# Kernel tuning notes

Measured on AMD Instinct MI355X. Metric: run time of the kernel, lower is better.

## Reference

```python
import math
import jax, jax.numpy as jnp
import numpy as np

D_MODEL = 1024
NUM_HEADS = 16
MAX_SEQ_LEN = 2048
THETA = 10000.0


def setup_inputs() -> dict:
    key = jax.random.key(0)
    ks = jax.random.split(key, 5)
    B, S, D = 2, 2048, D_MODEL
    std = math.sqrt(2.0 / (D + D))
    x = jax.random.normal(ks[0], (B, S, D), dtype=jnp.float32)
    wq = jax.random.normal(ks[1], (D, D), dtype=jnp.float32) * std
    wk = jax.random.normal(ks[2], (D, D), dtype=jnp.float32) * std
    wv = jax.random.normal(ks[3], (D, D), dtype=jnp.float32) * std
    wo = jax.random.normal(ks[4], (D, D), dtype=jnp.float32) * std
    return {"x": x, "wq": wq, "wk": wk, "wv": wv, "wo": wo}


def _rope_tables(seq_len: int, d_k: int):
    # angles[i, k] = i / theta^(2k/d_k), k over d_k//2 pairs
    inv_freq = 1.0 / (THETA ** (jnp.arange(0, d_k, 2, dtype=jnp.float32) / d_k))
    angles = jnp.arange(seq_len, dtype=jnp.float32)[:, None] * inv_freq[None, :]  # [S, d_k/2]
    return jnp.cos(angles), jnp.sin(angles)


def _apply_rope(x, cos, sin):
    # x: [..., S, d_k]; cos/sin: [S, d_k/2], broadcast over leading dims
    x_even = x[..., ::2]
    x_odd = x[..., 1::2]
    r_even = x_even * cos - x_odd * sin
    r_odd = x_even * sin + x_odd * cos
    return jnp.stack([r_even, r_odd], axis=-1).reshape(x.shape)


def reference(x, wq, wk, wv, wo):
    B, S, D = x.shape
    H = NUM_HEADS
    dk = D // H

    def split_heads(t):  # [B,S,D] -> [B,H,S,dk]
        return t.reshape(B, S, H, dk).transpose(0, 2, 1, 3)

    Q = split_heads(x @ wq.T)
    K = split_heads(x @ wk.T)
    V = split_heads(x @ wv.T)

    cos, sin = _rope_tables(S, dk)
    Q = _apply_rope(Q, cos, sin)
    K = _apply_rope(K, cos, sin)

    scores = jnp.einsum('bhqd,bhkd->bhqk', Q, K) / jnp.sqrt(jnp.float32(dk))
    mask = jnp.tril(jnp.ones((S, S), dtype=bool))  # causal: q can attend k <= q
    neg_inf = jnp.float32(-jnp.inf)
    scores = jnp.where(mask, scores, neg_inf)
    m = jnp.max(scores, axis=-1, keepdims=True)
    m = jnp.where(jnp.isinf(m), jnp.zeros_like(m), m)
    exp_scores = jnp.exp(scores - m)
    exp_scores = jnp.where(mask, exp_scores, 0.0)
    attn = exp_scores / (jnp.sum(exp_scores, axis=-1, keepdims=True) + 1e-9)
    out = jnp.einsum('bhqk,bhkd->bhqd', attn, V)  # [B,H,S,dk]
    out = out.transpose(0, 2, 1, 3).reshape(B, S, D)
    return out @ wo.T
```

## Files before the change

kernel.cpp:

```cpp
#include <hip/hip_runtime.h>
#include <stdint.h>

typedef unsigned short u16;
typedef unsigned int u32;
typedef __bf16 bf16x8 __attribute__((ext_vector_type(8)));
typedef float f32x4 __attribute__((ext_vector_type(4)));
typedef unsigned short u16x8 __attribute__((ext_vector_type(8)));

#define D_MODEL 1024
#define SEQ 2048
#define NH 16
#define DK 64
#define NROWS 4096

static __device__ __forceinline__ u16 f2bf(float f) {
  u32 u = __float_as_uint(f);
  u = (u + 0x7FFFu + ((u >> 16) & 1u)) >> 16;
  return (u16)u;
}
static __device__ __forceinline__ float bf2f(u16 h) {
  return __uint_as_float(((u32)h) << 16);
}
static __device__ __forceinline__ f32x4 mfma16(bf16x8 a, bf16x8 b, f32x4 c) {
  return __builtin_amdgcn_mfma_f32_16x16x32_bf16(a, b, c, 0, 0, 0);
}
static __device__ __forceinline__ void gload16(const void* g, void* l) {
  __builtin_amdgcn_global_load_lds(
      (const __attribute__((address_space(1))) void*)g,
      (__attribute__((address_space(3))) void*)l, 16, 0, 0);
}

static __device__ __forceinline__ float xor32_max(float x) {
#if __has_builtin(__builtin_amdgcn_permlane32_swap)
  u32 a = __float_as_uint(x), b = a;
  auto pr = __builtin_amdgcn_permlane32_swap(a, b, false, false);
  return fmaxf(__uint_as_float(pr[0]), __uint_as_float(pr[1]));
#else
  return fmaxf(x, __shfl_xor(x, 32));
#endif
}
static __device__ __forceinline__ float xor32_add(float x) {
#if __has_builtin(__builtin_amdgcn_permlane32_swap)
  u32 a = __float_as_uint(x), b = a;
  auto pr = __builtin_amdgcn_permlane32_swap(a, b, false, false);
  return __uint_as_float(pr[0]) + __uint_as_float(pr[1]);
#else
  return x + __shfl_xor(x, 32);
#endif
}

__global__ __launch_bounds__(256) void k_cast(
    const float* __restrict__ x, const float* __restrict__ wq,
    const float* __restrict__ wk, const float* __restrict__ wv,
    const float* __restrict__ wo, u16* __restrict__ xb, u16* __restrict__ wqb,
    u16* __restrict__ wkb, u16* __restrict__ wvb, u16* __restrict__ wob) {
  size_t e = ((size_t)blockIdx.x * 256 + threadIdx.x) * 8;
  const float* s;
  u16* d;
  size_t off;
  if (e < (size_t)NROWS * D_MODEL) {
    s = x; d = xb; off = e;
  } else {
    size_t r = e - (size_t)NROWS * D_MODEL;
    unsigned wi = (unsigned)(r >> 20);
    off = r & 1048575u;
    s = wi == 0 ? wq : wi == 1 ? wk : wi == 2 ? wv : wo;
    d = wi == 0 ? wqb : wi == 1 ? wkb : wi == 2 ? wvb : wob;
  }
  float4 a = *(const float4*)(s + off);
  float4 b = *(const float4*)(s + off + 4);
  u16x8 o;
  o[0] = f2bf(a.x); o[1] = f2bf(a.y); o[2] = f2bf(a.z); o[3] = f2bf(a.w);
  o[4] = f2bf(b.x); o[5] = f2bf(b.y); o[6] = f2bf(b.z); o[7] = f2bf(b.w);
  *(u16x8*)(d + off) = o;
}

__global__ __launch_bounds__(256) void k_tab(float* __restrict__ ct, float* __restrict__ st) {
  int i = blockIdx.x * 256 + threadIdx.x;
  int s = i >> 5, p = i & 31;
  double ang = (double)s * pow(10000.0, -(double)p / 32.0);
  ct[i] = (float)cos(ang);
  st[i] = (float)sin(ang);
}

template <bool MULTI, bool OUTF32>
__global__ __launch_bounds__(256, 1) void k_gemm(
    const u16* __restrict__ A, const u16* __restrict__ B0,
    const u16* __restrict__ B1, const u16* __restrict__ B2,
    u16* __restrict__ Cb, float* __restrict__ Cf, int ldc) {
  constexpr int K = 1024;
  const int mb = blockIdx.x, nb = blockIdx.y;
  const int tid = threadIdx.x;
  const int lane = tid & 63, w = tid >> 6;
  const int lq = lane & 15, lg = lane >> 4;
  const int wm = w >> 1, wn = w & 1;
  __shared__ __align__(16) u16 As[128 * 32];
  __shared__ __align__(16) u16 Bs[128 * 32];

  const u16* Bp;
  if (MULTI) {
    int sel = nb >> 3;
    Bp = sel == 0 ? B0 : (sel == 1 ? B1 : B2);
  } else {
    Bp = B0;
  }
  int nloc = MULTI ? (nb & 7) * 128 : nb * 128;
  const char* Ab = (const char*)A + (size_t)mb * 128 * 2048;
  const char* Bb = (const char*)Bp + (size_t)nloc * 2048;

  const int srow = tid >> 2;
  const int scb = (tid & 3) * 16;

  f32x4 zero4 = {0.f, 0.f, 0.f, 0.f};
  f32x4 acc[4][4];
#pragma unroll
  for (int i = 0; i < 4; ++i)
#pragma unroll
    for (int j = 0; j < 4; ++j) acc[i][j] = zero4;

  for (int k0 = 0; k0 < K; k0 += 32) {
#pragma unroll
    for (int c = 0; c < 2; ++c) {
      int o = c * 4096 + tid * 16;
      const char* ga = Ab + (size_t)(c * 64 + srow) * 2048 + k0 * 2 + scb;
      const char* gb = Bb + (size_t)(c * 64 + srow) * 2048 + k0 * 2 + scb;
      gload16(ga, (char*)As + o);
      gload16(gb, (char*)Bs + o);
    }
    __syncthreads();
    bf16x8 af[4], bfr[4];
#pragma unroll
    for (int i = 0; i < 4; ++i) {
      af[i] = *(const bf16x8*)((const char*)As + (wm * 64 + i * 16 + lq) * 64 + lg * 16);
      bfr[i] = *(const bf16x8*)((const char*)Bs + (wn * 64 + i * 16 + lq) * 64 + lg * 16);
    }
#pragma unroll
    for (int i = 0; i < 4; ++i)
#pragma unroll
      for (int j = 0; j < 4; ++j) acc[i][j] = mfma16(af[i], bfr[j], acc[i][j]);
    __syncthreads();
  }

#pragma unroll
  for (int i = 0; i < 4; ++i) {
#pragma unroll
    for (int r = 0; r < 4; ++r) {
      size_t rowg = (size_t)(mb * 128 + wm * 64 + i * 16 + lg * 4 + r);
#pragma unroll
      for (int j = 0; j < 4; ++j) {
        int colg = nb * 128 + wn * 64 + j * 16 + lq;
        if (OUTF32)
          Cf[rowg * ldc + colg] = acc[i][j][r];
        else
          Cb[rowg * ldc + colg] = f2bf(acc[i][j][r]);
      }
    }
  }
}

__global__ __launch_bounds__(256) void k_rope(const u16* __restrict__ qkv,
                                              const float* __restrict__ ct,
                                              const float* __restrict__ st,
                                              u16* __restrict__ qh, u16* __restrict__ kh) {
  int gi = blockIdx.x * 256 + threadIdx.x;
  int row = gi >> 7;
  int col = (gi & 127) << 3;
  int h = col >> 6, d0 = col & 63;
  int b = row >> 11, s = row & 2047;
  const int srcoff = blockIdx.y ? 1024 : 0;
  const float qs = blockIdx.y ? 1.0f : 0.18033688011112042f;
  u16x8 v = *(const u16x8*)(qkv + (size_t)row * 3072 + srcoff + col);
  const float* cp = ct + s * 32 + (d0 >> 1);
  const float* sp = st + s * 32 + (d0 >> 1);
  u16x8 o;
#pragma unroll
  for (int i = 0; i < 4; ++i) {
    float ev = bf2f(v[2 * i]), od = bf2f(v[2 * i + 1]);
    float c = cp[i], sn = sp[i];
    o[2 * i] = f2bf((ev * c - od * sn) * qs);
    o[2 * i + 1] = f2bf((ev * sn + od * c) * qs);
  }
  u16* dst = blockIdx.y ? kh : qh;
  *(u16x8*)(dst + (((size_t)(b * 16 + h) * SEQ + s) << 6) + d0) = o;
}

__global__ __launch_bounds__(256) void k_vtrans(const u16* __restrict__ qkv,
                                                u16* __restrict__ vt) {
  __shared__ __align__(16) u16 t[64][72];
  int sb = blockIdx.x, bh = blockIdx.y;
  int b = bh >> 4, h = bh & 15;
  int tid = threadIdx.x;
#pragma unroll
  for (int c = 0; c < 2; ++c) {
    int o = tid * 8 + c * 2048;
    int r = o >> 6, d = o & 63;
    u16x8 v = *(const u16x8*)(qkv + (size_t)(b * SEQ + sb * 64 + r) * 3072 + 2048 + h * 64 + d);
    *(u16x8*)&t[r][d] = v;
  }
  __syncthreads();
#pragma unroll
  for (int c = 0; c < 2; ++c) {
    int o = tid * 8 + c * 2048;
    int d = o >> 6, si = o & 63;
    u16x8 v;
#pragma unroll
    for (int j = 0; j < 8; ++j) v[j] = t[si + j][d];
    *(u16x8*)(vt + ((size_t)bh * 64 + d) * SEQ + sb * 64 + si) = v;
  }
}

static __device__ __forceinline__ void attn_tile(
    const u16* Kl, const u16* Vl, u16* Plw, int k0, int qrow, int lq, int lg,
    bf16x8 qf0, bf16x8 qf1, float& m_run, float& l_run, f32x4* accO, bool masked) {
  f32x4 zero4 = {0.f, 0.f, 0.f, 0.f};
  f32x4 sa[4];
  sa[0] = zero4; sa[1] = zero4; sa[2] = zero4; sa[3] = zero4;
  __builtin_amdgcn_s_setprio(1);
#pragma unroll
  for (int kt = 0; kt < 4; ++kt) {
    int krow = kt * 16 + lq;
    int base = krow * 128 + lg * 16;
    int swz = (krow & 7) << 4;
    bf16x8 kf0 = *(const bf16x8*)((const char*)Kl + (base ^ swz));
    bf16x8 kf1 = *(const bf16x8*)((const char*)Kl + ((base + 64) ^ swz));
    sa[kt] = mfma16(kf0, qf0, sa[kt]);
    sa[kt] = mfma16(kf1, qf1, sa[kt]);
  }
  __builtin_amdgcn_s_setprio(0);

  float p[16];
#pragma unroll
  for (int kt = 0; kt < 4; ++kt)
#pragma unroll
    for (int r = 0; r < 4; ++r) p[kt * 4 + r] = sa[kt][r];
  if (masked) {
#pragma unroll
    for (int kt = 0; kt < 4; ++kt)
#pragma unroll
      for (int r = 0; r < 4; ++r) {
        int key = k0 + kt * 16 + lg * 4 + r;
        if (key > qrow) p[kt * 4 + r] = -1e30f;
      }
  }
  float x0 = fmaxf(p[0], p[1]), x1 = fmaxf(p[2], p[3]);
  float x2 = fmaxf(p[4], p[5]), x3 = fmaxf(p[6], p[7]);
  float x4 = fmaxf(p[8], p[9]), x5 = fmaxf(p[10], p[11]);
  float x6 = fmaxf(p[12], p[13]), x7 = fmaxf(p[14], p[15]);
  x0 = fmaxf(x0, x1); x2 = fmaxf(x2, x3); x4 = fmaxf(x4, x5); x6 = fmaxf(x6, x7);
  x0 = fmaxf(x0, x2); x4 = fmaxf(x4, x6);
  float pm = fmaxf(x0, x4);
  pm = fmaxf(pm, __shfl_xor(pm, 16));
  pm = xor32_max(pm);
  const bool resc = __any(pm > m_run + 8.0f);
  float mnew = resc ? fmaxf(m_run, pm) : m_run;
#pragma unroll
  for (int i = 0; i < 16; ++i) p[i] = __builtin_amdgcn_exp2f(p[i] - mnew);
  float s0 = p[0] + p[1], s1 = p[2] + p[3], s2 = p[4] + p[5], s3 = p[6] + p[7];
  float s4 = p[8] + p[9], s5 = p[10] + p[11], s6 = p[12] + p[13], s7 = p[14] + p[15];
  s0 += s1; s2 += s3; s4 += s5; s6 += s7;
  s0 += s2; s4 += s6;
  float rs = s0 + s4;
  rs += __shfl_xor(rs, 16);
  rs = xor32_add(rs);
  if (resc) {
    float alpha = __builtin_amdgcn_exp2f(m_run - mnew);
    l_run = l_run * alpha + rs;
    m_run = mnew;
#pragma unroll
    for (int r = 0; r < 4; ++r) {
      float ar = __shfl(alpha, lg * 4 + r);
#pragma unroll
      for (int dt = 0; dt < 4; ++dt) accO[dt][r] *= ar;
    }
  } else {
    l_run += rs;
  }

  {
    int swz = (lq & 7) << 4;
#pragma unroll
    for (int kt = 0; kt < 4; ++kt) {
      u32 w0, w1;
      asm("v_cvt_pk_bf16_f32 %0, %1, %2"
          : "=v"(w0) : "v"(p[kt * 4 + 0]), "v"(p[kt * 4 + 1]));
      asm("v_cvt_pk_bf16_f32 %0, %1, %2"
          : "=v"(w1) : "v"(p[kt * 4 + 2]), "v"(p[kt * 4 + 3]));
      int a0 = (lq * 128 + (kt * 16 + lg * 4) * 2) ^ swz;
      int a1 = (lq * 128 + (kt * 16 + lg * 4 + 2) * 2) ^ swz;
      *(u32*)((char*)Plw + a0) = w0;
      *(u32*)((char*)Plw + a1) = w1;
    }
  }
  {
    int swz = (lq & 7) << 4;
    bf16x8 pa0 = *(const bf16x8*)((const char*)Plw + ((lq * 128 + lg * 16) ^ swz));
    bf16x8 pa1 = *(const bf16x8*)((const char*)Plw + ((lq * 128 + 64 + lg * 16) ^ swz));
    __builtin_amdgcn_s_setprio(1);
#pragma unroll
    for (int dt = 0; dt < 4; ++dt) {
      int vrow = dt * 16 + lq;
      int vb = vrow * 128 + lg * 16;
      int vs = (vrow & 7) << 4;
      bf16x8 v0 = *(const bf16x8*)((const char*)Vl + (vb ^ vs));
      bf16x8 v1 = *(const bf16x8*)((const char*)Vl + ((vb + 64) ^ vs));
      accO[dt] = mfma16(pa0, v0, accO[dt]);
      accO[dt] = mfma16(pa1, v1, accO[dt]);
    }
    __builtin_amdgcn_s_setprio(0);
  }
}

__global__ __launch_bounds__(256, 2) void k_attn(const u16* __restrict__ qh,
                                                 const u16* __restrict__ kh,
                                                 const u16* __restrict__ vt,
                                                 u16* __restrict__ ao) {
  const int qb1 = (int)blockIdx.x;
  const int qb2 = 31 - qb1;
  const int bh = blockIdx.y;
  const int tid = threadIdx.x;
  const int w = tid >> 6;
  const int lane = tid & 63;
  const int lq = lane & 15;
  const int lg = lane >> 4;

  __shared__ __align__(16) u16 Kd[2][2][64 * 64];
  __shared__ __align__(16) u16 Vd[2][2][64 * 64];
  __shared__ __align__(16) u16 Pl[4][16 * 64];

  const int qtop1 = qb1 * 64 + w * 16;
  const int qtop2 = qb2 * 64 + w * 16;
  const int qrow1 = qtop1 + lq;
  const int qrow2 = qtop2 + lq;

  const u16* qp1 = qh + ((size_t)bh * SEQ + qrow1) * DK + lg * 8;
  const u16* qp2 = qh + ((size_t)bh * SEQ + qrow2) * DK + lg * 8;
  bf16x8 qa0 = *(const bf16x8*)qp1;
  bf16x8 qa1 = *(const bf16x8*)(qp1 + 32);
  bf16x8 qc0 = *(const bf16x8*)qp2;
  bf16x8 qc1 = *(const bf16x8*)(qp2 + 32);

  f32x4 zero4 = {0.f, 0.f, 0.f, 0.f};
  f32x4 acc1[4], acc2[4];
#pragma unroll
  for (int dt = 0; dt < 4; ++dt) { acc1[dt] = zero4; acc2[dt] = zero4; }
  float m1 = -1e30f, l1 = 0.f, m2 = -1e30f, l2 = 0.f;

  const int nt1 = qb1 + 1;
  const int nt2 = qb2 + 1;
  const int NIT = (nt2 + 1) >> 1;

  const char* kb_ = (const char*)kh + (size_t)bh * SEQ * 128;
  const char* vb_ = (const char*)vt + (size_t)bh * DK * 4096;

#pragma unroll
  for (int s = 0; s < 2; ++s)
#pragma unroll
    for (int pass = 0; pass < 2; ++pass) {
      int chunk = pass * 256 + tid;
      int srow = chunk >> 3;
      int colb = ((chunk & 7) * 16) ^ ((srow & 7) << 4);
      gload16(kb_ + (size_t)(s * 64 + srow) * 128 + colb,
              (char*)Kd[0][s] + chunk * 16);
      gload16(vb_ + (size_t)srow * 4096 + (s * 64) * 2 + colb,
              (char*)Vd[0][s] + chunk * 16);
    }
  __syncthreads();

  for (int it = 0; it < NIT; ++it) {
    const int cur = it & 1;
    if (it + 1 < NIT) {
      int kb0 = (it + 1) * 128;
#pragma unroll
      for (int s = 0; s < 2; ++s)
#pragma unroll
        for (int pass = 0; pass < 2; ++pass) {
          int chunk = pass * 256 + tid;
          int srow = chunk >> 3;
          int colb = ((chunk & 7) * 16) ^ ((srow & 7) << 4);
          gload16(kb_ + (size_t)(kb0 + s * 64 + srow) * 128 + colb,
                  (char*)Kd[cur ^ 1][s] + chunk * 16);
          gload16(vb_ + (size_t)srow * 4096 + (kb0 + s * 64) * 2 + colb,
                  (char*)Vd[cur ^ 1][s] + chunk * 16);
        }
    }
#pragma unroll
    for (int s = 0; s < 2; ++s) {
      const int tsub = it * 2 + s;
      const int k0 = tsub * 64;
      if (tsub < nt1)
        attn_tile(Kd[cur][s], Vd[cur][s], Pl[w], k0, qrow1, lq, lg, qa0, qa1,
                  m1, l1, acc1, tsub == nt1 - 1);
      if (tsub < nt2)
        attn_tile(Kd[cur][s], Vd[cur][s], Pl[w], k0, qrow2, lq, lg, qc0, qc1,
                  m2, l2, acc2, tsub == nt2 - 1);
    }
    __syncthreads();
  }

  const int b = bh >> 4, h = bh & 15;
#pragma unroll
  for (int r = 0; r < 4; ++r) {
    float lr = __shfl(l1, lg * 4 + r);
    float inv = 1.f / (lr + 1e-9f);
    int qq = qtop1 + lg * 4 + r;
    u16* orow = ao + ((size_t)b * SEQ + qq) * D_MODEL + h * DK;
#pragma unroll
    for (int dt = 0; dt < 4; ++dt) orow[dt * 16 + lq] = f2bf(acc1[dt][r] * inv);
  }
#pragma unroll
  for (int r = 0; r < 4; ++r) {
    float lr = __shfl(l2, lg * 4 + r);
    float inv = 1.f / (lr + 1e-9f);
    int qq = qtop2 + lg * 4 + r;
    u16* orow = ao + ((size_t)b * SEQ + qq) * D_MODEL + h * DK;
#pragma unroll
    for (int dt = 0; dt < 4; ++dt) orow[dt * 16 + lq] = f2bf(acc2[dt][r] * inv);
  }
}

extern "C" void kernel_launch(void* const* d_in, const int* in_sizes, int n_in,
                              void* d_out, int out_size, void* d_ws, size_t ws_size,
                              hipStream_t stream) {
  const float* x = (const float*)d_in[0];
  const float* wq = (const float*)d_in[1];
  const float* wk = (const float*)d_in[2];
  const float* wv = (const float*)d_in[3];
  const float* wo = (const float*)d_in[4];
  float* out = (float*)d_out;
  char* ws = (char*)d_ws;

  u16* xb   = (u16*)(ws + 0);
  u16* wqb  = (u16*)(ws + 8388608);
  u16* wkb  = (u16*)(ws + 10485760);
  u16* wvb  = (u16*)(ws + 12582912);
  u16* wob  = (u16*)(ws + 14680064);
  u16* qkv  = (u16*)(ws + 16777216);
  u16* qhb  = (u16*)(ws + 41943040);
  u16* khb  = (u16*)(ws + 50331648);
  u16* vtb  = (u16*)(ws + 58720256);
  u16* aob  = (u16*)(ws + 67108864);
  float* ct = (float*)(ws + 75497472);
  float* st = (float*)(ws + 75759616);

  k_cast<<<4096, 256, 0, stream>>>(x, wq, wk, wv, wo, xb, wqb, wkb, wvb, wob);
  k_tab<<<256, 256, 0, stream>>>(ct, st);
  k_gemm<true, false><<<dim3(32, 24), 256, 0, stream>>>(xb, wqb, wkb, wvb, qkv, nullptr, 3072);
  k_rope<<<dim3(2048, 2), 256, 0, stream>>>(qkv, ct, st, qhb, khb);
  k_vtrans<<<dim3(32, 32), 256, 0, stream>>>(qkv, vtb);
  k_attn<<<dim3(16, 32), 256, 0, stream>>>(qhb, khb, vtb, aob);
  k_gemm<false, true><<<dim3(32, 8), 256, 0, stream>>>(aob, wob, nullptr, nullptr, nullptr, out, 1024);
}
```

Measured before the change: 126.2 us.

## Fuse RoPE and V transpose into QKV GEMM epilogue

The QKV projection GEMM now applies RoPE (with the Q scale) directly in its epilogue and writes Q/K in head-major layout. V is transposed through shared memory and written straight to the V^T buffer. This removes the intermediate qkv buffer along with the separate rope and vtrans kernels, saving two launches and a full write and read of qkv. The cost is extra LDS (a 128x136 transpose tile), strided scalar bf16 stores for Q/K, and a cos/sin table packed into float2.

```diff
diff --git a/kernel.cpp b/kernel.cpp
--- a/kernel.cpp
+++ b/kernel.cpp
@@ -75,19 +75,18 @@
   *(u16x8*)(d + off) = o;
 }
 
-__global__ __launch_bounds__(256) void k_tab(float* __restrict__ ct, float* __restrict__ st) {
+__global__ __launch_bounds__(256) void k_tab(float2* __restrict__ cs) {
   int i = blockIdx.x * 256 + threadIdx.x;
   int s = i >> 5, p = i & 31;
   double ang = (double)s * pow(10000.0, -(double)p / 32.0);
-  ct[i] = (float)cos(ang);
-  st[i] = (float)sin(ang);
-}
-
-template <bool MULTI, bool OUTF32>
-__global__ __launch_bounds__(256, 1) void k_gemm(
+  cs[i] = make_float2((float)cos(ang), (float)sin(ang));
+}
+
+__global__ __launch_bounds__(256, 1) void k_gemmqkv(
     const u16* __restrict__ A, const u16* __restrict__ B0,
     const u16* __restrict__ B1, const u16* __restrict__ B2,
-    u16* __restrict__ Cb, float* __restrict__ Cf, int ldc) {
+    const float2* __restrict__ cs, u16* __restrict__ qh,
+    u16* __restrict__ kh, u16* __restrict__ vt) {
   constexpr int K = 1024;
   const int mb = blockIdx.x, nb = blockIdx.y;
   const int tid = threadIdx.x;
@@ -96,15 +95,11 @@
   const int wm = w >> 1, wn = w & 1;
   __shared__ __align__(16) u16 As[128 * 32];
   __shared__ __align__(16) u16 Bs[128 * 32];
-
-  const u16* Bp;
-  if (MULTI) {
-    int sel = nb >> 3;
-    Bp = sel == 0 ? B0 : (sel == 1 ? B1 : B2);
-  } else {
-    Bp = B0;
-  }
-  int nloc = MULTI ? (nb & 7) * 128 : nb * 128;
+  __shared__ __align__(16) u16 Tr[128][136];
+
+  const int sel = nb >> 3;
+  const u16* Bp = sel == 0 ? B0 : (sel == 1 ? B1 : B2);
+  const int nloc = (nb & 7) * 128;
   const char* Ab = (const char*)A + (size_t)mb * 128 * 2048;
   const char* Bb = (const char*)Bp + (size_t)nloc * 2048;
 
@@ -141,6 +136,103 @@
     __syncthreads();
   }
 
+  if (sel < 2) {
+    u16* dst = sel ? kh : qh;
+    const float qs = sel ? 1.0f : 0.18033688011112042f;
+    const bool oddl = (lane & 1) != 0;
+#pragma unroll
+    for (int i = 0; i < 4; ++i) {
+#pragma unroll
+      for (int r = 0; r < 4; ++r) {
+        int rowg = mb * 128 + wm * 64 + i * 16 + lg * 4 + r;
+        int s = rowg & 2047, b = rowg >> 11;
+        const float2* csrow = cs + s * 32;
+#pragma unroll
+        for (int j = 0; j < 4; ++j) {
+          int colL = nloc + wn * 64 + j * 16 + lq;
+          float v = acc[i][j][r];
+          float pv = __shfl_xor(v, 1);
+          float2 c2 = csrow[(colL & 63) >> 1];
+          float t = pv * c2.y;
+          float res = (v * c2.x + (oddl ? t : -t)) * qs;
+          int h = colL >> 6, d = colL & 63;
+          dst[((size_t)(b * 16 + h) * 2048 + s) * 64 + d] = f2bf(res);
+        }
+      }
+    }
+  } else {
+#pragma unroll
+    for (int i = 0; i < 4; ++i)
+#pragma unroll
+      for (int j = 0; j < 4; ++j)
+#pragma unroll
+        for (int r = 0; r < 4; ++r) {
+          int cb = wn * 64 + j * 16 + lq;
+          int rb = wm * 64 + i * 16 + lg * 4 + r;
+          Tr[cb][rb] = f2bf(acc[i][j][r]);
+        }
+    __syncthreads();
+    const int b = mb >> 4;
+    const int s0 = (mb & 15) * 128 + (tid & 1) * 64;
+    const int d128 = tid >> 1;
+    const int h = (nb & 7) * 2 + (d128 >> 6);
+    const int d = d128 & 63;
+    u16* vrow = vt + ((size_t)(b * 16 + h) * 64 + d) * 2048 + s0;
+    const u16* trow = &Tr[d128][(tid & 1) * 64];
+#pragma unroll
+    for (int c = 0; c < 8; ++c)
+      *(u16x8*)(vrow + c * 8) = *(const u16x8*)(trow + c * 8);
+  }
+}
+
+__global__ __launch_bounds__(256, 1) void k_gemm(
+    const u16* __restrict__ A, const u16* __restrict__ B0,
+    float* __restrict__ Cf, int ldc) {
+  constexpr int K = 1024;
+  const int mb = blockIdx.x, nb = blockIdx.y;
+  const int tid = threadIdx.x;
+  const int lane = tid & 63, w = tid >> 6;
+  const int lq = lane & 15, lg = lane >> 4;
+  const int wm = w >> 1, wn = w & 1;
+  __shared__ __align__(16) u16 As[128 * 32];
+  __shared__ __align__(16) u16 Bs[128 * 32];
+
+  const char* Ab = (const char*)A + (size_t)mb * 128 * 2048;
+  const char* Bb = (const char*)B0 + (size_t)(nb * 128) * 2048;
+
+  const int srow = tid >> 2;
+  const int scb = (tid & 3) * 16;
+
+  f32x4 zero4 = {0.f, 0.f, 0.f, 0.f};
+  f32x4 acc[4][4];
+#pragma unroll
+  for (int i = 0; i < 4; ++i)
+#pragma unroll
+    for (int j = 0; j < 4; ++j) acc[i][j] = zero4;
+
+  for (int k0 = 0; k0 < K; k0 += 32) {
+#pragma unroll
+    for (int c = 0; c < 2; ++c) {
+      int o = c * 4096 + tid * 16;
+      const char* ga = Ab + (size_t)(c * 64 + srow) * 2048 + k0 * 2 + scb;
+      const char* gb = Bb + (size_t)(c * 64 + srow) * 2048 + k0 * 2 + scb;
+      gload16(ga, (char*)As + o);
+      gload16(gb, (char*)Bs + o);
+    }
+    __syncthreads();
+    bf16x8 af[4], bfr[4];
+#pragma unroll
+    for (int i = 0; i < 4; ++i) {
+      af[i] = *(const bf16x8*)((const char*)As + (wm * 64 + i * 16 + lq) * 64 + lg * 16);
+      bfr[i] = *(const bf16x8*)((const char*)Bs + (wn * 64 + i * 16 + lq) * 64 + lg * 16);
+    }
+#pragma unroll
+    for (int i = 0; i < 4; ++i)
+#pragma unroll
+      for (int j = 0; j < 4; ++j) acc[i][j] = mfma16(af[i], bfr[j], acc[i][j]);
+    __syncthreads();
+  }
+
 #pragma unroll
   for (int i = 0; i < 4; ++i) {
 #pragma unroll
@@ -149,63 +241,9 @@
 #pragma unroll
       for (int j = 0; j < 4; ++j) {
         int colg = nb * 128 + wn * 64 + j * 16 + lq;
-        if (OUTF32)
-          Cf[rowg * ldc + colg] = acc[i][j][r];
-        else
-          Cb[rowg * ldc + colg] = f2bf(acc[i][j][r]);
+        Cf[rowg * ldc + colg] = acc[i][j][r];
       }
     }
-  }
-}
-
-__global__ __launch_bounds__(256) void k_rope(const u16* __restrict__ qkv,
-                                              const float* __restrict__ ct,
-                                              const float* __restrict__ st,
-                                              u16* __restrict__ qh, u16* __restrict__ kh) {
-  int gi = blockIdx.x * 256 + threadIdx.x;
-  int row = gi >> 7;
-  int col = (gi & 127) << 3;
-  int h = col >> 6, d0 = col & 63;
-  int b = row >> 11, s = row & 2047;
-  const int srcoff = blockIdx.y ? 1024 : 0;
-  const float qs = blockIdx.y ? 1.0f : 0.18033688011112042f;
-  u16x8 v = *(const u16x8*)(qkv + (size_t)row * 3072 + srcoff + col);
-  const float* cp = ct + s * 32 + (d0 >> 1);
-  const float* sp = st + s * 32 + (d0 >> 1);
-  u16x8 o;
-#pragma unroll
-  for (int i = 0; i < 4; ++i) {
-    float ev = bf2f(v[2 * i]), od = bf2f(v[2 * i + 1]);
-    float c = cp[i], sn = sp[i];
-    o[2 * i] = f2bf((ev * c - od * sn) * qs);
-    o[2 * i + 1] = f2bf((ev * sn + od * c) * qs);
-  }
-  u16* dst = blockIdx.y ? kh : qh;
-  *(u16x8*)(dst + (((size_t)(b * 16 + h) * SEQ + s) << 6) + d0) = o;
-}
-
-__global__ __launch_bounds__(256) void k_vtrans(const u16* __restrict__ qkv,
-                                                u16* __restrict__ vt) {
-  __shared__ __align__(16) u16 t[64][72];
-  int sb = blockIdx.x, bh = blockIdx.y;
-  int b = bh >> 4, h = bh & 15;
-  int tid = threadIdx.x;
-#pragma unroll
-  for (int c = 0; c < 2; ++c) {
-    int o = tid * 8 + c * 2048;
-    int r = o >> 6, d = o & 63;
-    u16x8 v = *(const u16x8*)(qkv + (size_t)(b * SEQ + sb * 64 + r) * 3072 + 2048 + h * 64 + d);
-    *(u16x8*)&t[r][d] = v;
-  }
-  __syncthreads();
-#pragma unroll
-  for (int c = 0; c < 2; ++c) {
-    int o = tid * 8 + c * 2048;
-    int d = o >> 6, si = o & 63;
-    u16x8 v;
-#pragma unroll
-    for (int j = 0; j < 8; ++j) v[j] = t[si + j][d];
-    *(u16x8*)(vt + ((size_t)bh * 64 + d) * SEQ + sb * 64 + si) = v;
   }
 }
 
@@ -429,24 +467,20 @@
   float* out = (float*)d_out;
   char* ws = (char*)d_ws;
 
-  u16* xb   = (u16*)(ws + 0);
-  u16* wqb  = (u16*)(ws + 8388608);
-  u16* wkb  = (u16*)(ws + 10485760);
-  u16* wvb  = (u16*)(ws + 12582912);
-  u16* wob  = (u16*)(ws + 14680064);
-  u16* qkv  = (u16*)(ws + 16777216);
-  u16* qhb  = (u16*)(ws + 41943040);
-  u16* khb  = (u16*)(ws + 50331648);
-  u16* vtb  = (u16*)(ws + 58720256);
-  u16* aob  = (u16*)(ws + 67108864);
-  float* ct = (float*)(ws + 75497472);
-  float* st = (float*)(ws + 75759616);
+  u16* xb    = (u16*)(ws + 0);
+  u16* wqb   = (u16*)(ws + 8388608);
+  u16* wkb   = (u16*)(ws + 10485760);
+  u16* wvb   = (u16*)(ws + 12582912);
+  u16* wob   = (u16*)(ws + 14680064);
+  u16* qhb   = (u16*)(ws + 41943040);
+  u16* khb   = (u16*)(ws + 50331648);
+  u16* vtb   = (u16*)(ws + 58720256);
+  u16* aob   = (u16*)(ws + 67108864);
+  float2* cs = (float2*)(ws + 75497472);
 
   k_cast<<<4096, 256, 0, stream>>>(x, wq, wk, wv, wo, xb, wqb, wkb, wvb, wob);
-  k_tab<<<256, 256, 0, stream>>>(ct, st);
-  k_gemm<true, false><<<dim3(32, 24), 256, 0, stream>>>(xb, wqb, wkb, wvb, qkv, nullptr, 3072);
-  k_rope<<<dim3(2048, 2), 256, 0, stream>>>(qkv, ct, st, qhb, khb);
-  k_vtrans<<<dim3(32, 32), 256, 0, stream>>>(qkv, vtb);
+  k_tab<<<256, 256, 0, stream>>>(cs);
+  k_gemmqkv<<<dim3(32, 24), 256, 0, stream>>>(xb, wqb, wkb, wvb, cs, qhb, khb, vtb);
   k_attn<<<dim3(16, 32), 256, 0, stream>>>(qhb, khb, vtb, aob);
-  k_gemm<false, true><<<dim3(32, 8), 256, 0, stream>>>(aob, wob, nullptr, nullptr, nullptr, out, 1024);
-}
+  k_gemm<<<dim3(32, 8), 256, 0, stream>>>(aob, wob, out, 1024);
+}
```

Result: slower. 131.8 us (+4.5%).

## Deepen GEMM K-tile to 64 with XOR-swizzled LDS and split output GEMM tiles

Applied to the files above, without the earlier changes.

The QKV GEMM now stages a 64-wide K slice per iteration, which halves the number of barrier pairs. Its LDS layout is XOR-swizzled so that fragment reads avoid bank conflicts. The output projection gets its own kernel with a 128x64 tile and two blocks per CU, doubling its grid from 256 to 512 blocks to fill the GPU better. In exchange, LDS use per block doubles, and the narrower output tile re-reads A more often.

```diff
diff --git a/kernel.cpp b/kernel.cpp
--- a/kernel.cpp
+++ b/kernel.cpp
@@ -83,34 +83,25 @@
   st[i] = (float)sin(ang);
 }
 
-template <bool MULTI, bool OUTF32>
-__global__ __launch_bounds__(256, 1) void k_gemm(
+__global__ __launch_bounds__(256, 1) void k_gemm3(
     const u16* __restrict__ A, const u16* __restrict__ B0,
     const u16* __restrict__ B1, const u16* __restrict__ B2,
-    u16* __restrict__ Cb, float* __restrict__ Cf, int ldc) {
+    u16* __restrict__ Cb) {
   constexpr int K = 1024;
   const int mb = blockIdx.x, nb = blockIdx.y;
   const int tid = threadIdx.x;
   const int lane = tid & 63, w = tid >> 6;
   const int lq = lane & 15, lg = lane >> 4;
   const int wm = w >> 1, wn = w & 1;
-  __shared__ __align__(16) u16 As[128 * 32];
-  __shared__ __align__(16) u16 Bs[128 * 32];
-
-  const u16* Bp;
-  if (MULTI) {
-    int sel = nb >> 3;
-    Bp = sel == 0 ? B0 : (sel == 1 ? B1 : B2);
-  } else {
-    Bp = B0;
-  }
-  int nloc = MULTI ? (nb & 7) * 128 : nb * 128;
+  __shared__ __align__(16) u16 As[128 * 64];
+  __shared__ __align__(16) u16 Bs[128 * 64];
+
+  const int sel = nb >> 3;
+  const u16* Bp = sel == 0 ? B0 : (sel == 1 ? B1 : B2);
+  const int nloc = (nb & 7) * 128;
   const char* Ab = (const char*)A + (size_t)mb * 128 * 2048;
   const char* Bb = (const char*)Bp + (size_t)nloc * 2048;
 
-  const int srow = tid >> 2;
-  const int scb = (tid & 3) * 16;
-
   f32x4 zero4 = {0.f, 0.f, 0.f, 0.f};
   f32x4 acc[4][4];
 #pragma unroll
@@ -118,26 +109,35 @@
 #pragma unroll
     for (int j = 0; j < 4; ++j) acc[i][j] = zero4;
 
-  for (int k0 = 0; k0 < K; k0 += 32) {
-#pragma unroll
-    for (int c = 0; c < 2; ++c) {
-      int o = c * 4096 + tid * 16;
-      const char* ga = Ab + (size_t)(c * 64 + srow) * 2048 + k0 * 2 + scb;
-      const char* gb = Bb + (size_t)(c * 64 + srow) * 2048 + k0 * 2 + scb;
-      gload16(ga, (char*)As + o);
-      gload16(gb, (char*)Bs + o);
+  for (int k0 = 0; k0 < K; k0 += 64) {
+#pragma unroll
+    for (int c = 0; c < 4; ++c) {
+      int ch = c * 256 + tid;
+      int srow = ch >> 3;
+      int scb = ((ch & 7) * 16) ^ ((srow & 7) << 4);
+      const char* ga = Ab + (size_t)srow * 2048 + k0 * 2 + scb;
+      const char* gb = Bb + (size_t)srow * 2048 + k0 * 2 + scb;
+      gload16(ga, (char*)As + ch * 16);
+      gload16(gb, (char*)Bs + ch * 16);
     }
     __syncthreads();
-    bf16x8 af[4], bfr[4];
-#pragma unroll
-    for (int i = 0; i < 4; ++i) {
-      af[i] = *(const bf16x8*)((const char*)As + (wm * 64 + i * 16 + lq) * 64 + lg * 16);
-      bfr[i] = *(const bf16x8*)((const char*)Bs + (wn * 64 + i * 16 + lq) * 64 + lg * 16);
-    }
-#pragma unroll
-    for (int i = 0; i < 4; ++i)
-#pragma unroll
-      for (int j = 0; j < 4; ++j) acc[i][j] = mfma16(af[i], bfr[j], acc[i][j]);
+#pragma unroll
+    for (int ks = 0; ks < 2; ++ks) {
+      bf16x8 af[4], bfr[4];
+#pragma unroll
+      for (int i = 0; i < 4; ++i) {
+        int ra = wm * 64 + i * 16 + lq;
+        int rb = wn * 64 + i * 16 + lq;
+        af[i] = *(const bf16x8*)((const char*)As +
+                                 ra * 128 + ((ks * 64 + lg * 16) ^ ((ra & 7) << 4)));
+        bfr[i] = *(const bf16x8*)((const char*)Bs +
+                                  rb * 128 + ((ks * 64 + lg * 16) ^ ((rb & 7) << 4)));
+      }
+#pragma unroll
+      for (int i = 0; i < 4; ++i)
+#pragma unroll
+        for (int j = 0; j < 4; ++j) acc[i][j] = mfma16(af[i], bfr[j], acc[i][j]);
+    }
     __syncthreads();
   }
 
@@ -149,10 +149,7 @@
 #pragma unroll
       for (int j = 0; j < 4; ++j) {
         int colg = nb * 128 + wn * 64 + j * 16 + lq;
-        if (OUTF32)
-          Cf[rowg * ldc + colg] = acc[i][j][r];
-        else
-          Cb[rowg * ldc + colg] = f2bf(acc[i][j][r]);
+        Cb[rowg * 3072 + colg] = f2bf(acc[i][j][r]);
       }
     }
   }
@@ -209,6 +206,76 @@
   }
 }
 
+__global__ __launch_bounds__(256, 2) void k_gemmo(const u16* __restrict__ A,
+                                                  const u16* __restrict__ B0,
+                                                  float* __restrict__ Cf) {
+  constexpr int K = 1024;
+  const int mb = blockIdx.x, nb = blockIdx.y;
+  const int tid = threadIdx.x;
+  const int lane = tid & 63, w = tid >> 6;
+  const int lq = lane & 15, lg = lane >> 4;
+  const int wm = w >> 1, wn = w & 1;
+  __shared__ __align__(16) u16 As[128 * 64];
+  __shared__ __align__(16) u16 Bs[64 * 64];
+
+  const char* Ab = (const char*)A + (size_t)mb * 128 * 2048;
+  const char* Bb = (const char*)B0 + (size_t)(nb * 64) * 2048;
+
+  f32x4 zero4 = {0.f, 0.f, 0.f, 0.f};
+  f32x4 acc[4][2];
+#pragma unroll
+  for (int i = 0; i < 4; ++i) {
+    acc[i][0] = zero4; acc[i][1] = zero4;
+  }
+
+  for (int k0 = 0; k0 < K; k0 += 64) {
+#pragma unroll
+    for (int c = 0; c < 4; ++c) {
+      int ch = c * 256 + tid;
+      int srow = ch >> 3;
+      int scb = ((ch & 7) * 16) ^ ((srow & 7) << 4);
+      gload16(Ab + (size_t)srow * 2048 + k0 * 2 + scb, (char*)As + ch * 16);
+      if (c < 2)
+        gload16(Bb + (size_t)srow * 2048 + k0 * 2 + scb, (char*)Bs + ch * 16);
+    }
+    __syncthreads();
+#pragma unroll
+    for (int ks = 0; ks < 2; ++ks) {
+      bf16x8 af[4], bfr[2];
+#pragma unroll
+      for (int i = 0; i < 4; ++i) {
+        int ra = wm * 64 + i * 16 + lq;
+        af[i] = *(const bf16x8*)((const char*)As +
+                                 ra * 128 + ((ks * 64 + lg * 16) ^ ((ra & 7) << 4)));
+      }
+#pragma unroll
+      for (int j = 0; j < 2; ++j) {
+        int rb = wn * 32 + j * 16 + lq;
+        bfr[j] = *(const bf16x8*)((const char*)Bs +
+                                  rb * 128 + ((ks * 64 + lg * 16) ^ ((rb & 7) << 4)));
+      }
+#pragma unroll
+      for (int i = 0; i < 4; ++i)
+#pragma unroll
+        for (int j = 0; j < 2; ++j) acc[i][j] = mfma16(af[i], bfr[j], acc[i][j]);
+    }
+    __syncthreads();
+  }
+
+#pragma unroll
+  for (int i = 0; i < 4; ++i) {
+#pragma unroll
+    for (int r = 0; r < 4; ++r) {
+      size_t rowg = (size_t)(mb * 128 + wm * 64 + i * 16 + lg * 4 + r);
+#pragma unroll
+      for (int j = 0; j < 2; ++j) {
+        int colg = nb * 64 + wn * 32 + j * 16 + lq;
+        Cf[rowg * 1024 + colg] = acc[i][j][r];
+      }
+    }
+  }
+}
+
 static __device__ __forceinline__ void attn_tile(
     const u16* Kl, const u16* Vl, u16* Plw, int k0, int qrow, int lq, int lg,
     bf16x8 qf0, bf16x8 qf1, float& m_run, float& l_run, f32x4* accO, bool masked) {
@@ -444,9 +511,9 @@
 
   k_cast<<<4096, 256, 0, stream>>>(x, wq, wk, wv, wo, xb, wqb, wkb, wvb, wob);
   k_tab<<<256, 256, 0, stream>>>(ct, st);
-  k_gemm<true, false><<<dim3(32, 24), 256, 0, stream>>>(xb, wqb, wkb, wvb, qkv, nullptr, 3072);
+  k_gemm3<<<dim3(32, 24), 256, 0, stream>>>(xb, wqb, wkb, wvb, qkv);
   k_rope<<<dim3(2048, 2), 256, 0, stream>>>(qkv, ct, st, qhb, khb);
   k_vtrans<<<dim3(32, 32), 256, 0, stream>>>(qkv, vtb);
   k_attn<<<dim3(16, 32), 256, 0, stream>>>(qhb, khb, vtb, aob);
-  k_gemm<false, true><<<dim3(32, 8), 256, 0, stream>>>(aob, wob, nullptr, nullptr, nullptr, out, 1024);
-}
+  k_gemmo<<<dim3(32, 16), 256, 0, stream>>>(aob, wob, out);
+}
```

Result: faster. 115.2 us (-8.7%).
